# Kernel optimization log

Measured on AMD Instinct MI355X. Metric: run time of the kernel, lower is better.

The kernel has to match this reference:

```python
import jax, jax.numpy as jnp
import numpy as np


def setup_inputs() -> dict:
    key = jax.random.key(0)
    k1, k2, k3 = jax.random.split(key, 3)
    d_model, L, batch = 1024, 8192, 2
    h = jax.random.normal(k1, (d_model, L), dtype=jnp.float32)
    x = jax.random.normal(k2, (batch, d_model, L), dtype=jnp.float32)
    B = jax.random.normal(k3, (d_model, 1), dtype=jnp.float32)
    return {"h": h, "x": x, "B": B}


def reference(h, x, B):
    # L = max(x.shape[-1], h.shape[-1]); static under jit
    L = max(x.shape[-1], h.shape[-1])
    n = 2 * L  # zero-pad to 2L for linear (non-circular) convolution
    # torch norm='forward': rfft scaled by 1/n, irfft unscaled
    h_f = jnp.fft.rfft(h, n=n, norm="forward")          # (d, L+1) complex
    x_f = jnp.fft.rfft(x, n=n)                            # (b, d, L+1) complex
    y = jnp.fft.irfft(h_f * x_f, n=n, norm="forward")[..., :L]
    y = y + x * B  # residual with per-channel gate, B broadcasts over L
    return y.astype(h.dtype)
```

## Files before the change

kernel.cpp:

```cpp
#include <hip/hip_runtime.h>


typedef float v2f __attribute__((ext_vector_type(2)));

#define L_SEQ   8192
#define N_FFT   16384
#define D_MODEL 1024
#define NTH     1024

#define SWZ(i) ((i) ^ (((i) >> 4) & 15))

#define C16_1 0.92387953251128675613f
#define S16_1 0.38268343236508977173f
#define C16_2 0.70710678118654752440f

__device__ __forceinline__ void wave_fence() {
    asm volatile("s_waitcnt lgkmcnt(0)" ::: "memory");
    __builtin_amdgcn_sched_barrier(0);
}

__device__ __forceinline__ v2f mkv2(float a, float b) { v2f r; r.x = a; r.y = b; return r; }

__device__ __forceinline__ v2f cmul(v2f a, v2f b) {
    const v2f brot = mkv2(-b.y, b.x);
    return a.x * b + a.y * brot;
}
__device__ __forceinline__ v2f cmulc(v2f a, float re, float im) {
    const v2f arot = mkv2(-a.y, a.x);
    return re * a + im * arot;
}

__device__ __forceinline__ v2f hw_cis(float rev) {
    return mkv2(__builtin_amdgcn_cosf(rev), __builtin_amdgcn_sinf(rev));
}

__device__ __forceinline__ unsigned bf2pack(float re, float im) {
    unsigned r;
    asm("v_cvt_pk_bf16_f32 %0, %1, %2" : "=v"(r) : "v"(re), "v"(im));
    return r;
}
__device__ __forceinline__ unsigned bf2pack2(v2f v) { return bf2pack(v.x, v.y); }

__device__ __forceinline__ v2f bf2unpack(unsigned p) {
    return mkv2(__uint_as_float(p << 16), __uint_as_float(p & 0xffff0000u));
}

template <int S>
__device__ __forceinline__ void bfly4(v2f& r0, v2f& r1, v2f& r2, v2f& r3) {
    const v2f t0 = r0 + r2;
    const v2f t1 = r0 - r2;
    const v2f t2 = r1 + r3;
    const v2f t3 = r1 - r3;
    r0 = t0 + t2;
    r2 = t0 - t2;
    if (S < 0) {
        r1 = mkv2(t1.x + t3.y, t1.y - t3.x);
        r3 = mkv2(t1.x - t3.y, t1.y + t3.x);
    } else {
        r1 = mkv2(t1.x - t3.y, t1.y + t3.x);
        r3 = mkv2(t1.x + t3.y, t1.y - t3.x);
    }
}

template <int S>
__device__ __forceinline__ void dft16_mid_twiddle(v2f a[16]) {
    const float s = (float)S;
    a[5]  = cmulc(a[5],   C16_1,  s * S16_1);
    a[9]  = cmulc(a[9],   C16_2,  s * C16_2);
    a[13] = cmulc(a[13],  S16_1,  s * C16_1);
    a[6]  = cmulc(a[6],   C16_2,  s * C16_2);
    a[10] = mkv2(-s * a[10].y, s * a[10].x);
    a[14] = cmulc(a[14], -C16_2,  s * C16_2);
    a[7]  = cmulc(a[7],   S16_1,  s * C16_1);
    a[11] = cmulc(a[11], -C16_2,  s * C16_2);
    a[15] = cmulc(a[15], -C16_1, -s * S16_1);
}

template <int S>
__device__ __forceinline__ void dft16(v2f a[16]) {
    bfly4<S>(a[0], a[4], a[8],  a[12]);
    bfly4<S>(a[1], a[5], a[9],  a[13]);
    bfly4<S>(a[2], a[6], a[10], a[14]);
    bfly4<S>(a[3], a[7], a[11], a[15]);
    dft16_mid_twiddle<S>(a);
    bfly4<S>(a[0],  a[1],  a[2],  a[3]);
    bfly4<S>(a[4],  a[5],  a[6],  a[7]);
    bfly4<S>(a[8],  a[9],  a[10], a[11]);
    bfly4<S>(a[12], a[13], a[14], a[15]);
}

template <int S>
__device__ __forceinline__ void inner4_halfzero(v2f a[16]) {
#pragma unroll
    for (int c = 0; c < 4; ++c) {
        const v2f p = a[c], q = a[c + 4];
        a[c]      = p + q;
        a[c + 8]  = p - q;
        if (S < 0) {
            a[c + 4]  = mkv2(p.x + q.y, p.y - q.x);
            a[c + 12] = mkv2(p.x - q.y, p.y + q.x);
        } else {
            a[c + 4]  = mkv2(p.x - q.y, p.y + q.x);
            a[c + 12] = mkv2(p.x + q.y, p.y - q.x);
        }
    }
}

__device__ __forceinline__ void fwd_stage1_finish(unsigned* __restrict__ zz,
                                                  const int tid, v2f a[16]) {
    dft16_mid_twiddle<-1>(a);
    bfly4<-1>(a[0],  a[1],  a[2],  a[3]);
    bfly4<-1>(a[4],  a[5],  a[6],  a[7]);
    bfly4<-1>(a[8],  a[9],  a[10], a[11]);
    bfly4<-1>(a[12], a[13], a[14], a[15]);
    const v2f w1 = hw_cis(-(float)tid * (1.0f / 16384.0f));
    zz[SWZ(tid)] = bf2pack2(a[0]);
    v2f wc = w1;
#pragma unroll
    for (int L = 1; L < 16; ++L) {
        const int P = ((L & 3) << 2) | (L >> 2);
        zz[SWZ(tid + (L << 10))] = bf2pack2(cmul(a[P], wc));
        wc = cmul(wc, w1);
    }
    __syncthreads();
}

template <int S, int LQ>
__device__ __forceinline__ void fft16_stage_bf(unsigned* __restrict__ zz, const int tid) {
    const int q = 1 << LQ;
    const int j = tid & (q - 1);
    const int base = ((tid >> LQ) << (LQ + 4)) | j;
    const v2f w1 = hw_cis((float)S * (float)j / (float)(1 << (LQ + 4)));
    v2f a[16];
    if (S < 0) {
#pragma unroll
        for (int m = 0; m < 16; ++m) a[m] = bf2unpack(zz[SWZ(base + m * q)]);
        dft16<S>(a);
        zz[SWZ(base)] = bf2pack2(a[0]);
        v2f wc = w1;
#pragma unroll
        for (int L = 1; L < 16; ++L) {
            const int P = ((L & 3) << 2) | (L >> 2);
            zz[SWZ(base + L * q)] = bf2pack2(cmul(a[P], wc));
            wc = cmul(wc, w1);
        }
    } else {
#pragma unroll
        for (int k = 0; k < 16; ++k) a[k] = bf2unpack(zz[SWZ(base + k * q)]);
        v2f wc = w1;
#pragma unroll
        for (int k = 1; k < 16; ++k) { a[k] = cmul(a[k], wc); wc = cmul(wc, w1); }
        dft16<S>(a);
#pragma unroll
        for (int M = 0; M < 16; ++M) {
            const int P = ((M & 3) << 2) | (M >> 2);
            zz[SWZ(base + M * q)] = bf2pack2(a[P]);
        }
    }
}

__global__ void __launch_bounds__(NTH) fftconv_filter_kernel(
        const float* __restrict__ h, const float* __restrict__ Bg,
        unsigned* __restrict__ Hws) {
    extern __shared__ unsigned zz[];
    const int d = blockIdx.x;
    const int tid = threadIdx.x;
    const int w = tid >> 6, l = tid & 63;
    const float invn = 1.0f / (float)N_FFT;
    const float Bs = Bg[d] * invn;

    {
        const float* hrow = h + (size_t)d * L_SEQ;
        v2f a[16];
#pragma unroll
        for (int m = 0; m < 8; ++m)
            a[m] = mkv2(hrow[tid + (m << 10)], 0.0f);
        inner4_halfzero<-1>(a);
        fwd_stage1_finish(zz, tid, a);
    }
    fft16_stage_bf<-1, 6>(zz, tid);
    wave_fence();
    fft16_stage_bf<-1, 2>(zz, tid);
    wave_fence();

    unsigned* Hrow = Hws + (size_t)d * N_FFT;
#pragma unroll
    for (int r = 0; r < 4; ++r) {
        const int qi = (w << 8) + (r << 6) + l;
        const int b = qi << 2;
        v2f a0 = bf2unpack(zz[SWZ(b)]);
        v2f a1 = bf2unpack(zz[SWZ(b + 1)]);
        v2f a2 = bf2unpack(zz[SWZ(b + 2)]);
        v2f a3 = bf2unpack(zz[SWZ(b + 3)]);
        bfly4<-1>(a0, a1, a2, a3);
        ((uint4*)Hrow)[qi] = make_uint4(
            bf2pack(a0.x * invn + Bs, a0.y * invn),
            bf2pack(a1.x * invn + Bs, a1.y * invn),
            bf2pack(a2.x * invn + Bs, a2.y * invn),
            bf2pack(a3.x * invn + Bs, a3.y * invn));
    }
}

__global__ void __launch_bounds__(NTH) fftconv_conv_kernel(
        const float* __restrict__ x, const unsigned* __restrict__ Hws,
        float* __restrict__ y) {
    extern __shared__ unsigned zz[];
    const int d = blockIdx.x;
    const int tid = threadIdx.x;
    const int w = tid >> 6, l = tid & 63;

    const float* x0 = x + (size_t)d * L_SEQ;
    const float* x1 = x + (size_t)(D_MODEL + d) * L_SEQ;

    {
        v2f a[16];
#pragma unroll
        for (int m = 0; m < 8; ++m) {
            const int idx = tid + (m << 10);
            a[m] = mkv2(x0[idx], x1[idx]);
        }
        inner4_halfzero<-1>(a);
        fwd_stage1_finish(zz, tid, a);
    }
    fft16_stage_bf<-1, 6>(zz, tid);
    wave_fence();

    const uint4* Hp = (const uint4*)(Hws + (size_t)d * N_FFT);
    const int qbase = (w << 8) + l;
    const uint4 hp0 = Hp[qbase];
    const uint4 hp1 = Hp[qbase + 64];
    const uint4 hp2 = Hp[qbase + 128];
    const uint4 hp3 = Hp[qbase + 192];

    fft16_stage_bf<-1, 2>(zz, tid);
    wave_fence();

#pragma unroll
    for (int r = 0; r < 4; ++r) {
        const int b = ((w << 8) + (r << 6) + l) << 2;
        const int p0 = SWZ(b), p1 = SWZ(b + 1), p2 = SWZ(b + 2), p3 = SWZ(b + 3);
        v2f a0 = bf2unpack(zz[p0]);
        v2f a1 = bf2unpack(zz[p1]);
        v2f a2 = bf2unpack(zz[p2]);
        v2f a3 = bf2unpack(zz[p3]);
        bfly4<-1>(a0, a1, a2, a3);
        const uint4 hp = (r == 0) ? hp0 : (r == 1) ? hp1 : (r == 2) ? hp2 : hp3;
        a0 = cmul(a0, bf2unpack(hp.x));
        a1 = cmul(a1, bf2unpack(hp.y));
        a2 = cmul(a2, bf2unpack(hp.z));
        a3 = cmul(a3, bf2unpack(hp.w));
        bfly4<+1>(a0, a1, a2, a3);
        zz[p0] = bf2pack2(a0);
        zz[p1] = bf2pack2(a1);
        zz[p2] = bf2pack2(a2);
        zz[p3] = bf2pack2(a3);
    }
    wave_fence();

    fft16_stage_bf<+1, 2>(zz, tid);
    wave_fence();
    fft16_stage_bf<+1, 6>(zz, tid);
    __syncthreads();

    {
        v2f a[16];
#pragma unroll
        for (int k = 0; k < 16; ++k) a[k] = bf2unpack(zz[SWZ(tid + (k << 10))]);
        const v2f w1 = hw_cis((float)tid * (1.0f / 16384.0f));
        v2f wc = w1;
#pragma unroll
        for (int k = 1; k < 16; ++k) { a[k] = cmul(a[k], wc); wc = cmul(wc, w1); }
        bfly4<+1>(a[0], a[4], a[8],  a[12]);
        bfly4<+1>(a[1], a[5], a[9],  a[13]);
        bfly4<+1>(a[2], a[6], a[10], a[14]);
        bfly4<+1>(a[3], a[7], a[11], a[15]);
        dft16_mid_twiddle<+1>(a);
        float* y0 = y + (size_t)d * L_SEQ;
        float* y1 = y + (size_t)(D_MODEL + d) * L_SEQ;
#pragma unroll
        for (int g = 0; g < 4; ++g) {
            const v2f b0 = a[4*g], b1 = a[4*g+1], b2 = a[4*g+2], b3 = a[4*g+3];
            const v2f t0 = b0 + b2;
            const v2f t1 = b0 - b2;
            const v2f t2 = b1 + b3;
            const v2f t3 = b1 - b3;
            const v2f r0 = t0 + t2;
            const v2f r1 = mkv2(t1.x - t3.y, t1.y + t3.x);
            const int q0 = tid + (g << 10);
            const int q1 = tid + ((g + 4) << 10);
            y0[q0] = r0.x; y1[q0] = r0.y;
            y0[q1] = r1.x; y1[q1] = r1.y;
        }
    }
}

extern "C" void kernel_launch(void* const* d_in, const int* in_sizes, int n_in,
                              void* d_out, int out_size, void* d_ws, size_t ws_size,
                              hipStream_t stream) {
    const float* h = (const float*)d_in[0];
    const float* x = (const float*)d_in[1];
    const float* B = (const float*)d_in[2];
    float* y = (float*)d_out;
    unsigned* Hws = (unsigned*)d_ws;

    const size_t lds_bytes = (size_t)N_FFT * sizeof(unsigned);

    fftconv_filter_kernel<<<dim3(D_MODEL), dim3(NTH), lds_bytes, stream>>>(h, B, Hws);
    fftconv_conv_kernel<<<dim3(D_MODEL), dim3(NTH), lds_bytes, stream>>>(x, Hws, y);
}
```

Before: 105.3 us.

## Replace XOR swizzle with padded LDS layout and relax intra-wave fences

Switches the shared-memory layout from an XOR swizzle to padding (one extra word per 32), with addresses computed as base plus constant offsets so the compiler can fold them into immediate offsets. Replaces the s_waitcnt/sched_barrier wave fences with plain compiler memory fences, and swaps the hardware bf16 pack instruction for an add-and-permute rounding sequence. It also moves the first radix-16 stage after the filter prefetch loads so global latency overlaps LDS work. The risks are extra LDS usage, different bf16 rounding (round-half-up instead of round-to-nearest-even), and correctness relying on the compiler honoring LDS ordering within a wave without explicit waitcnt.

```diff
diff --git a/kernel.cpp b/kernel.cpp
--- a/kernel.cpp
+++ b/kernel.cpp
@@ -7,16 +7,14 @@
 #define N_FFT   16384
 #define D_MODEL 1024
 #define NTH     1024
-
-#define SWZ(i) ((i) ^ (((i) >> 4) & 15))
+#define LDS_U32 (N_FFT + (N_FFT >> 5))
 
 #define C16_1 0.92387953251128675613f
 #define S16_1 0.38268343236508977173f
 #define C16_2 0.70710678118654752440f
 
-__device__ __forceinline__ void wave_fence() {
-    asm volatile("s_waitcnt lgkmcnt(0)" ::: "memory");
-    __builtin_amdgcn_sched_barrier(0);
+__device__ __forceinline__ void compiler_fence() {
+    asm volatile("" ::: "memory");
 }
 
 __device__ __forceinline__ v2f mkv2(float a, float b) { v2f r; r.x = a; r.y = b; return r; }
@@ -35,9 +33,9 @@
 }
 
 __device__ __forceinline__ unsigned bf2pack(float re, float im) {
-    unsigned r;
-    asm("v_cvt_pk_bf16_f32 %0, %1, %2" : "=v"(r) : "v"(re), "v"(im));
-    return r;
+    const unsigned r = __float_as_uint(re) + 0x8000u;
+    const unsigned i = __float_as_uint(im) + 0x8000u;
+    return __builtin_amdgcn_perm(i, r, 0x07060302u);
 }
 __device__ __forceinline__ unsigned bf2pack2(v2f v) { return bf2pack(v.x, v.y); }
 
@@ -113,13 +111,14 @@
     bfly4<-1>(a[4],  a[5],  a[6],  a[7]);
     bfly4<-1>(a[8],  a[9],  a[10], a[11]);
     bfly4<-1>(a[12], a[13], a[14], a[15]);
+    const int pb1 = tid + (tid >> 5);
     const v2f w1 = hw_cis(-(float)tid * (1.0f / 16384.0f));
-    zz[SWZ(tid)] = bf2pack2(a[0]);
+    zz[pb1] = bf2pack2(a[0]);
     v2f wc = w1;
 #pragma unroll
     for (int L = 1; L < 16; ++L) {
         const int P = ((L & 3) << 2) | (L >> 2);
-        zz[SWZ(tid + (L << 10))] = bf2pack2(cmul(a[P], wc));
+        zz[pb1 + 1056 * L] = bf2pack2(cmul(a[P], wc));
         wc = cmul(wc, w1);
     }
     __syncthreads();
@@ -130,23 +129,31 @@
     const int q = 1 << LQ;
     const int j = tid & (q - 1);
     const int base = ((tid >> LQ) << (LQ + 4)) | j;
+    const int pbase = base + (base >> 5);
     const v2f w1 = hw_cis((float)S * (float)j / (float)(1 << (LQ + 4)));
     v2f a[16];
     if (S < 0) {
 #pragma unroll
-        for (int m = 0; m < 16; ++m) a[m] = bf2unpack(zz[SWZ(base + m * q)]);
+        for (int m = 0; m < 16; ++m) {
+            const int off = (LQ == 6) ? 66 * m : 4 * m + (m >> 3);
+            a[m] = bf2unpack(zz[pbase + off]);
+        }
         dft16<S>(a);
-        zz[SWZ(base)] = bf2pack2(a[0]);
+        zz[pbase] = bf2pack2(a[0]);
         v2f wc = w1;
 #pragma unroll
         for (int L = 1; L < 16; ++L) {
             const int P = ((L & 3) << 2) | (L >> 2);
-            zz[SWZ(base + L * q)] = bf2pack2(cmul(a[P], wc));
+            const int off = (LQ == 6) ? 66 * L : 4 * L + (L >> 3);
+            zz[pbase + off] = bf2pack2(cmul(a[P], wc));
             wc = cmul(wc, w1);
         }
     } else {
 #pragma unroll
-        for (int k = 0; k < 16; ++k) a[k] = bf2unpack(zz[SWZ(base + k * q)]);
+        for (int k = 0; k < 16; ++k) {
+            const int off = (LQ == 6) ? 66 * k : 4 * k + (k >> 3);
+            a[k] = bf2unpack(zz[pbase + off]);
+        }
         v2f wc = w1;
 #pragma unroll
         for (int k = 1; k < 16; ++k) { a[k] = cmul(a[k], wc); wc = cmul(wc, w1); }
@@ -154,7 +161,8 @@
 #pragma unroll
         for (int M = 0; M < 16; ++M) {
             const int P = ((M & 3) << 2) | (M >> 2);
-            zz[SWZ(base + M * q)] = bf2pack2(a[P]);
+            const int off = (LQ == 6) ? 66 * M : 4 * M + (M >> 3);
+            zz[pbase + off] = bf2pack2(a[P]);
         }
     }
 }
@@ -179,19 +187,19 @@
         fwd_stage1_finish(zz, tid, a);
     }
     fft16_stage_bf<-1, 6>(zz, tid);
-    wave_fence();
+    compiler_fence();
     fft16_stage_bf<-1, 2>(zz, tid);
-    wave_fence();
+    compiler_fence();
 
     unsigned* Hrow = Hws + (size_t)d * N_FFT;
 #pragma unroll
     for (int r = 0; r < 4; ++r) {
         const int qi = (w << 8) + (r << 6) + l;
-        const int b = qi << 2;
-        v2f a0 = bf2unpack(zz[SWZ(b)]);
-        v2f a1 = bf2unpack(zz[SWZ(b + 1)]);
-        v2f a2 = bf2unpack(zz[SWZ(b + 2)]);
-        v2f a3 = bf2unpack(zz[SWZ(b + 3)]);
+        const int pb = 4 * qi + (qi >> 3);
+        v2f a0 = bf2unpack(zz[pb]);
+        v2f a1 = bf2unpack(zz[pb + 1]);
+        v2f a2 = bf2unpack(zz[pb + 2]);
+        v2f a3 = bf2unpack(zz[pb + 3]);
         bfly4<-1>(a0, a1, a2, a3);
         ((uint4*)Hrow)[qi] = make_uint4(
             bf2pack(a0.x * invn + Bs, a0.y * invn),
@@ -222,8 +230,6 @@
         inner4_halfzero<-1>(a);
         fwd_stage1_finish(zz, tid, a);
     }
-    fft16_stage_bf<-1, 6>(zz, tid);
-    wave_fence();
 
     const uint4* Hp = (const uint4*)(Hws + (size_t)d * N_FFT);
     const int qbase = (w << 8) + l;
@@ -232,17 +238,19 @@
     const uint4 hp2 = Hp[qbase + 128];
     const uint4 hp3 = Hp[qbase + 192];
 
+    fft16_stage_bf<-1, 6>(zz, tid);
+    compiler_fence();
     fft16_stage_bf<-1, 2>(zz, tid);
-    wave_fence();
+    compiler_fence();
 
 #pragma unroll
     for (int r = 0; r < 4; ++r) {
-        const int b = ((w << 8) + (r << 6) + l) << 2;
-        const int p0 = SWZ(b), p1 = SWZ(b + 1), p2 = SWZ(b + 2), p3 = SWZ(b + 3);
-        v2f a0 = bf2unpack(zz[p0]);
-        v2f a1 = bf2unpack(zz[p1]);
-        v2f a2 = bf2unpack(zz[p2]);
-        v2f a3 = bf2unpack(zz[p3]);
+        const int qi = (w << 8) + (r << 6) + l;
+        const int pb = 4 * qi + (qi >> 3);
+        v2f a0 = bf2unpack(zz[pb]);
+        v2f a1 = bf2unpack(zz[pb + 1]);
+        v2f a2 = bf2unpack(zz[pb + 2]);
+        v2f a3 = bf2unpack(zz[pb + 3]);
         bfly4<-1>(a0, a1, a2, a3);
         const uint4 hp = (r == 0) ? hp0 : (r == 1) ? hp1 : (r == 2) ? hp2 : hp3;
         a0 = cmul(a0, bf2unpack(hp.x));
@@ -250,22 +258,23 @@
         a2 = cmul(a2, bf2unpack(hp.z));
         a3 = cmul(a3, bf2unpack(hp.w));
         bfly4<+1>(a0, a1, a2, a3);
-        zz[p0] = bf2pack2(a0);
-        zz[p1] = bf2pack2(a1);
-        zz[p2] = bf2pack2(a2);
-        zz[p3] = bf2pack2(a3);
-    }
-    wave_fence();
+        zz[pb]     = bf2pack2(a0);
+        zz[pb + 1] = bf2pack2(a1);
+        zz[pb + 2] = bf2pack2(a2);
+        zz[pb + 3] = bf2pack2(a3);
+    }
+    compiler_fence();
 
     fft16_stage_bf<+1, 2>(zz, tid);
-    wave_fence();
+    compiler_fence();
     fft16_stage_bf<+1, 6>(zz, tid);
     __syncthreads();
 
     {
+        const int pb1 = tid + (tid >> 5);
         v2f a[16];
 #pragma unroll
-        for (int k = 0; k < 16; ++k) a[k] = bf2unpack(zz[SWZ(tid + (k << 10))]);
+        for (int k = 0; k < 16; ++k) a[k] = bf2unpack(zz[pb1 + 1056 * k]);
         const v2f w1 = hw_cis((float)tid * (1.0f / 16384.0f));
         v2f wc = w1;
 #pragma unroll
@@ -303,7 +312,7 @@
     float* y = (float*)d_out;
     unsigned* Hws = (unsigned*)d_ws;
 
-    const size_t lds_bytes = (size_t)N_FFT * sizeof(unsigned);
+    const size_t lds_bytes = (size_t)LDS_U32 * sizeof(unsigned);
 
     fftconv_filter_kernel<<<dim3(D_MODEL), dim3(NTH), lds_bytes, stream>>>(h, B, Hws);
     fftconv_conv_kernel<<<dim3(D_MODEL), dim3(NTH), lds_bytes, stream>>>(x, Hws, y);
```

Result: no change. 106.5 us (+1.1%).
